# Kernel optimization log

Measured on AMD Instinct MI355X. Metric: run time of the kernel, lower is better.

Reference implementation:

```python
import jax, jax.numpy as jnp
import numpy as np

K, T, D, S, A, C, H = 128, 64, 128, 512, 4, 16, 512
N_LEAVES = 128
TEMP = 1.0          # sample_merge_temp
EPS_SQRT = 1e-4     # distances.EPSILON ** 0.5 with EPSILON = 1e-8
_SQ_EPS = 1e-12     # numerical guard inside sqrt (diagonal of pairwise dists is 0)


def setup_inputs() -> dict:
    key = jax.random.key(0)
    ks = jax.random.split(key, 11)
    leaf_counts_Kxt = jax.random.randint(ks[0], (K, T), 1, 5)
    embeddings_KxtxD = jax.random.normal(ks[1], (K, T, D), jnp.float32)
    log_felsensteins_KxtxSxA = jax.random.normal(ks[2], (K, T, S, A), jnp.float32)
    site_positions_SxC = jax.random.uniform(ks[3], (S, C), jnp.float32)
    W1 = jax.random.normal(ks[4], (2 * D, H), jnp.float32) / jnp.sqrt(2.0 * D)
    b1 = jnp.zeros((H,), jnp.float32)
    W2 = jax.random.normal(ks[5], (H, D), jnp.float32) / jnp.sqrt(1.0 * H)
    b2 = jnp.zeros((D,), jnp.float32)
    gumbel_Kxtt = jax.random.gumbel(ks[6], (K, T * T), jnp.float32)
    u1_K = jax.random.uniform(ks[7], (K,), jnp.float32, minval=1e-6, maxval=1.0)
    u2_K = jax.random.uniform(ks[8], (K,), jnp.float32, minval=1e-6, maxval=1.0)
    return {
        "N": N_LEAVES,
        "leaf_counts_Kxt": leaf_counts_Kxt,
        "embeddings_KxtxD": embeddings_KxtxD,
        "log_felsensteins_KxtxSxA": log_felsensteins_KxtxSxA,
        "site_positions_SxC": site_positions_SxC,
        "W1": W1, "b1": b1, "W2": W2, "b2": b2,
        "gumbel_Kxtt": gumbel_Kxtt, "u1_K": u1_K, "u2_K": u2_K,
    }


def _merge_encoder(c1_KxD, c2_KxD, W1, b1, W2, b2):
    # MLP merge encoder: MLP(concat(child1, child2)) -> parent embedding
    h = jax.nn.relu(jnp.concatenate([c1_KxD, c2_KxD], axis=-1) @ W1 + b1)
    return h @ W2 + b2


def reference(N, leaf_counts_Kxt, embeddings_KxtxD, log_felsensteins_KxtxSxA,
              site_positions_SxC, W1, b1, W2, b2, gumbel_Kxtt, u1_K, u2_K):
    Kp, t = leaf_counts_Kxt.shape
    ar = jnp.arange(Kp)

    # --- pairwise distances over all t*t subtree pairs per particle ---
    diff_Kxtxtxd = embeddings_KxtxD[:, :, None, :] - embeddings_KxtxD[:, None, :, :]
    pd_Kxtxt = jnp.sqrt(jnp.sum(diff_Kxtxtxd * diff_Kxtxtxd, axis=-1) + _SQ_EPS)
    merge_log_weights_Kxtxt = -pd_Kxtxt / TEMP
    # diagonal_scatter(-inf): forbid self-merges
    eye = jnp.eye(t, dtype=bool)[None]
    merge_log_weights_Kxtxt = jnp.where(eye, -jnp.inf, merge_log_weights_Kxtxt)

    # --- categorical merge sampling (gumbel-max with pre-drawn noise) ---
    flat_Kxtt = merge_log_weights_Kxtxt.reshape(Kp, t * t)
    sample_K = jnp.argmax(flat_Kxtt + gumbel_Kxtt, axis=1)
    idx1_K = sample_K // t
    idx2_K = sample_K % t
    log_merge_prob_K = (flat_Kxtt[ar, sample_K] + jnp.log(2.0)
                        - jax.scipy.special.logsumexp(flat_Kxtt, axis=1))

    # --- merged embedding ---
    child1_KxD = embeddings_KxtxD[ar, idx1_K]
    child2_KxD = embeddings_KxtxD[ar, idx2_K]
    embedding_KxD = _merge_encoder(child1_KxD, child2_KxD, W1, b1, W2, b2)

    # --- branch lengths sampled from Exp(rate = 1/(dist + eps)) ---
    d1_K = jnp.sqrt(jnp.sum((child1_KxD - embedding_KxD) ** 2, axis=-1) + _SQ_EPS)
    d2_K = jnp.sqrt(jnp.sum((child2_KxD - embedding_KxD) ** 2, axis=-1) + _SQ_EPS)
    rate1_K = 1.0 / (d1_K + EPS_SQRT)
    rate2_K = 1.0 / (d2_K + EPS_SQRT)
    branch1_K = -(1.0 / rate1_K) * jnp.log(u1_K)
    branch2_K = -(1.0 / rate2_K) * jnp.log(u2_K)
    log_branch1_prior_K = jnp.log(rate1_K) - rate1_K * branch1_K
    log_branch2_prior_K = jnp.log(rate2_K) - rate2_K * branch2_K

    log_v_plus_K = log_merge_prob_K + log_branch1_prior_K + log_branch2_prior_K

    # --- over-counting correction ---
    ones_K = jnp.sum(leaf_counts_Kxt == 1, axis=1)
    ones_K = ones_K - (leaf_counts_Kxt[ar, idx1_K] == 1).astype(ones_K.dtype)
    ones_K = ones_K - (leaf_counts_Kxt[ar, idx2_K] == 1).astype(ones_K.dtype)
    log_v_minus_K = jnp.log((N - ones_K).astype(jnp.float32))

    return (idx1_K, idx2_K, branch1_K, branch2_K, embedding_KxD,
            log_v_plus_K, log_v_minus_K)
```

## Files before the change

kernel.cpp:

```cpp
#include <hip/hip_runtime.h>
#include <math.h>

#define Kp 128
#define Tn 64
#define Dn 128
#define Hn 512
#define ETS 68

__global__ __launch_bounds__(256, 1) void ep_kernel(
    const int*   __restrict__ Nptr,
    const int*   __restrict__ leaf,
    const float* __restrict__ emb,
    const float* __restrict__ W1,
    const float* __restrict__ b1,
    const float* __restrict__ W2,
    const float* __restrict__ b2,
    const float* __restrict__ gum,
    const float* __restrict__ u1,
    const float* __restrict__ u2,
    float* __restrict__ out)
{
    const int k    = blockIdx.x;
    const int tid  = threadIdx.x;
    const int lane = tid & 63;
    const int wid  = tid >> 6;

    __shared__ float ET[Dn * ETS];
    __shared__ float xs[256];
    __shared__ float hsh[Hn];
    __shared__ float buf[1024];
    __shared__ float nI[Tn];
    __shared__ float sBest[4]; __shared__ int sIdx[4]; __shared__ float sW[4];
    __shared__ float sSum[4];
    __shared__ float sD1[4]; __shared__ float sD2[4];
    __shared__ int   sOnes;
    __shared__ int   fIdx; __shared__ float fW;
    __shared__ float embs[Dn];

    if (tid < 64) {
        int lc = leaf[k * Tn + tid];
        unsigned long long m = __ballot(lc == 1);
        if (tid == 0) sOnes = __popcll(m);
    }

    const int tx = tid & 15;
    const int ty = tid >> 4;
    float4 ev[8];
    {
        const float4* src = (const float4*)(emb + (size_t)k * Tn * Dn);
        #pragma unroll
        for (int it = 0; it < 8; ++it) ev[it] = src[tid + it * 256];
    }
    float4 g4[4];
    {
        const float* gk = gum + (size_t)k * (Tn * Tn);
        #pragma unroll
        for (int r = 0; r < 4; ++r) g4[r] = *(const float4*)&gk[(4 * ty + r) * Tn + 4 * tx];
    }

    #pragma unroll
    for (int it = 0; it < 8; ++it) {
        int f4 = tid + it * 256;
        int e0 = f4 * 4;
        int i = e0 >> 7;
        int d = e0 & 127;
        ET[(d + 0) * ETS + i] = ev[it].x;
        ET[(d + 1) * ETS + i] = ev[it].y;
        ET[(d + 2) * ETS + i] = ev[it].z;
        ET[(d + 3) * ETS + i] = ev[it].w;
    }
    __syncthreads();

    float acc[4][4] = {};
    #pragma unroll 4
    for (int d = 0; d < Dn; ++d) {
        float4 a = *(const float4*)&ET[d * ETS + 4 * ty];
        float4 b = *(const float4*)&ET[d * ETS + 4 * tx];
        float ar[4] = {a.x, a.y, a.z, a.w};
        float br[4] = {b.x, b.y, b.z, b.w};
        #pragma unroll
        for (int r = 0; r < 4; ++r)
            #pragma unroll
            for (int c = 0; c < 4; ++c)
                acc[r][c] += ar[r] * br[c];
    }
    if (tx == ty) {
        #pragma unroll
        for (int c = 0; c < 4; ++c) nI[4 * tx + c] = acc[c][c];
    }
    __syncthreads();

    float es = 0.0f;
    float best = -INFINITY, bestW = 0.0f;
    int   bestIdx = 0;
    #pragma unroll
    for (int r = 0; r < 4; ++r) {
        int i = 4 * ty + r;
        float ni = nI[i];
        float gv[4] = {g4[r].x, g4[r].y, g4[r].z, g4[r].w};
        #pragma unroll
        for (int c = 0; c < 4; ++c) {
            int j = 4 * tx + c;
            float pd2 = ni + nI[j] - 2.0f * acc[r][c];
            pd2 = fmaxf(pd2, 0.0f) + 1e-12f;
            float wv = (i == j) ? -INFINITY : -sqrtf(pd2);
            es += expf(wv);
            float wg = wv + gv[c];
            int idx = i * Tn + j;
            if (wg > best || (wg == best && idx < bestIdx)) {
                best = wg; bestIdx = idx; bestW = wv;
            }
        }
    }

    #pragma unroll
    for (int off = 32; off > 0; off >>= 1) {
        float ob = __shfl_down(best, off);
        int   oi = __shfl_down(bestIdx, off);
        float ow = __shfl_down(bestW, off);
        float oe = __shfl_down(es, off);
        if (ob > best || (ob == best && oi < bestIdx)) { best = ob; bestIdx = oi; bestW = ow; }
        es += oe;
    }
    if (lane == 0) { sBest[wid] = best; sIdx[wid] = bestIdx; sW[wid] = bestW; sSum[wid] = es; }
    __syncthreads();
    if (tid == 0) {
        best = sBest[0]; bestIdx = sIdx[0]; bestW = sW[0];
        #pragma unroll
        for (int q = 1; q < 4; ++q) {
            if (sBest[q] > best || (sBest[q] == best && sIdx[q] < bestIdx)) {
                best = sBest[q]; bestIdx = sIdx[q]; bestW = sW[q];
            }
        }
        fIdx = bestIdx; fW = bestW;
    }
    __syncthreads();

    const int i1 = fIdx >> 6;
    const int i2 = fIdx & 63;

    xs[tid] = (tid < 128) ? ET[tid * ETS + i1] : ET[(tid - 128) * ETS + i2];
    __syncthreads();

    {
        const int j0 = 4 * (tid & 127);
        const int ih = tid >> 7;
        const float* W1r = W1 + j0;
        float a0 = 0.0f, a1 = 0.0f, a2 = 0.0f, a3 = 0.0f;
        const int ibase = ih * 128;
        #pragma unroll 4
        for (int i = ibase; i < ibase + 128; i += 4) {
            float4 x  = *(const float4*)&xs[i];
            float4 w0 = *(const float4*)&W1r[(size_t)(i + 0) * Hn];
            float4 w1 = *(const float4*)&W1r[(size_t)(i + 1) * Hn];
            float4 w2 = *(const float4*)&W1r[(size_t)(i + 2) * Hn];
            float4 w3 = *(const float4*)&W1r[(size_t)(i + 3) * Hn];
            a0 += x.x * w0.x + x.y * w1.x + x.z * w2.x + x.w * w3.x;
            a1 += x.x * w0.y + x.y * w1.y + x.z * w2.y + x.w * w3.y;
            a2 += x.x * w0.z + x.y * w1.z + x.z * w2.z + x.w * w3.z;
            a3 += x.x * w0.w + x.y * w1.w + x.z * w2.w + x.w * w3.w;
        }
        *(float4*)&buf[ih * Hn + j0] = make_float4(a0, a1, a2, a3);
    }
    __syncthreads();
    {
        int j = tid;
        hsh[j] = fmaxf(buf[j] + buf[Hn + j] + b1[j], 0.0f);
        j = tid + 256;
        hsh[j] = fmaxf(buf[j] + buf[Hn + j] + b1[j], 0.0f);
    }
    __syncthreads();

    {
        const int jh  = tid >> 5;
        const int dd4 = 4 * (tid & 31);
        float a0 = 0.0f, a1 = 0.0f, a2 = 0.0f, a3 = 0.0f;
        const int jbase = jh * 64;
        #pragma unroll 4
        for (int j = jbase; j < jbase + 64; j += 4) {
            float4 h4 = *(const float4*)&hsh[j];
            float4 w0 = *(const float4*)&W2[(size_t)(j + 0) * Dn + dd4];
            float4 w1 = *(const float4*)&W2[(size_t)(j + 1) * Dn + dd4];
            float4 w2 = *(const float4*)&W2[(size_t)(j + 2) * Dn + dd4];
            float4 w3 = *(const float4*)&W2[(size_t)(j + 3) * Dn + dd4];
            a0 += h4.x * w0.x + h4.y * w1.x + h4.z * w2.x + h4.w * w3.x;
            a1 += h4.x * w0.y + h4.y * w1.y + h4.z * w2.y + h4.w * w3.y;
            a2 += h4.x * w0.z + h4.y * w1.z + h4.z * w2.z + h4.w * w3.z;
            a3 += h4.x * w0.w + h4.y * w1.w + h4.z * w2.w + h4.w * w3.w;
        }
        *(float4*)&buf[jh * Dn + dd4] = make_float4(a0, a1, a2, a3);
    }
    __syncthreads();
    if (tid < 128) {
        float e = b2[tid];
        #pragma unroll
        for (int q = 0; q < 8; ++q) e += buf[q * Dn + tid];
        embs[tid] = e;
        out[4 * Kp + k * Dn + tid] = e;
    }
    __syncthreads();

    float v1 = 0.0f, v2 = 0.0f;
    if (tid < 128) {
        float e  = embs[tid];
        float q1 = xs[tid] - e;        v1 = q1 * q1;
        float q2 = xs[128 + tid] - e;  v2 = q2 * q2;
    }
    #pragma unroll
    for (int off = 32; off > 0; off >>= 1) {
        v1 += __shfl_down(v1, off);
        v2 += __shfl_down(v2, off);
    }
    if (lane == 0) { sD1[wid] = v1; sD2[wid] = v2; }
    __syncthreads();

    if (tid == 0) {
        float s1 = sD1[0] + sD1[1] + sD1[2] + sD1[3];
        float s2 = sD2[0] + sD2[1] + sD2[2] + sD2[3];
        float d1 = sqrtf(s1 + 1e-12f);
        float d2 = sqrtf(s2 + 1e-12f);
        float rate1 = 1.0f / (d1 + 1e-4f);
        float rate2 = 1.0f / (d2 + 1e-4f);
        float u1v = u1[k], u2v = u2[k];
        float branch1 = -(1.0f / rate1) * logf(u1v);
        float branch2 = -(1.0f / rate2) * logf(u2v);
        float lbp1 = logf(rate1) - rate1 * branch1;
        float lbp2 = logf(rate2) - rate2 * branch2;
        float ssum = sSum[0] + sSum[1] + sSum[2] + sSum[3];
        float lse  = logf(ssum);
        float lmp  = fW + 0.69314718055994531f - lse;
        float lvp  = lmp + lbp1 + lbp2;
        int lc1 = leaf[k * Tn + i1];
        int lc2 = leaf[k * Tn + i2];
        int ones = sOnes - (lc1 == 1 ? 1 : 0) - (lc2 == 1 ? 1 : 0);
        float lvm = logf((float)(Nptr[0] - ones));

        out[k]                       = (float)i1;
        out[Kp + k]                  = (float)i2;
        out[2 * Kp + k]              = branch1;
        out[3 * Kp + k]              = branch2;
        out[4 * Kp + Kp * Dn + k]      = lvp;
        out[4 * Kp + Kp * Dn + Kp + k] = lvm;
    }
}

extern "C" void kernel_launch(void* const* d_in, const int* in_sizes, int n_in,
                              void* d_out, int out_size, void* d_ws, size_t ws_size,
                              hipStream_t stream) {
    const int*   Nptr = (const int*)  d_in[0];
    const int*   leaf = (const int*)  d_in[1];
    const float* emb  = (const float*)d_in[2];
    const float* W1   = (const float*)d_in[5];
    const float* b1   = (const float*)d_in[6];
    const float* W2   = (const float*)d_in[7];
    const float* b2   = (const float*)d_in[8];
    const float* gum  = (const float*)d_in[9];
    const float* u1   = (const float*)d_in[10];
    const float* u2   = (const float*)d_in[11];
    float* out = (float*)d_out;

    ep_kernel<<<Kp, 256, 0, stream>>>(Nptr, leaf, emb, W1, b1, W2, b2, gum, u1, u2, out);
}
```

Before: 131.2 us.

## Exploit Gram symmetry, split-K across 512 threads, swizzle shared-memory transpose

Doubles the block to 512 threads. The Gram matrix is computed only for upper-triangle and diagonal 4x4 tiles, using symmetry, with split-K partial sums reduced through shared scratch. The transposed embedding tile uses an XOR-like swizzled index to cut bank conflicts. Both MLP layers also split their reduction dimension across more threads. This halves the pairwise FLOPs and raises parallelism per particle, at the cost of extra shared-memory reductions, barriers and uneven work across threads.

Result: slower. 134.8 us (+2.7%).

```diff
diff --git a/kernel.cpp b/kernel.cpp
--- a/kernel.cpp
+++ b/kernel.cpp
@@ -7,7 +7,11 @@
 #define Hn 512
 #define ETS 68
 
-__global__ __launch_bounds__(256, 1) void ep_kernel(
+__device__ __forceinline__ int etIdx(int d, int i) {
+    return d * ETS + (((((i >> 2) + (d >> 2)) & 15) << 2) | (i & 3));
+}
+
+__global__ __launch_bounds__(512, 1) void ep_kernel(
     const int*   __restrict__ Nptr,
     const int*   __restrict__ leaf,
     const float* __restrict__ emb,
@@ -26,89 +30,175 @@
     const int wid  = tid >> 6;
 
     __shared__ float ET[Dn * ETS];
+    __shared__ float scratch[6016];
     __shared__ float xs[256];
     __shared__ float hsh[Hn];
-    __shared__ float buf[1024];
     __shared__ float nI[Tn];
-    __shared__ float sBest[4]; __shared__ int sIdx[4]; __shared__ float sW[4];
-    __shared__ float sSum[4];
-    __shared__ float sD1[4]; __shared__ float sD2[4];
+    __shared__ float embs[Dn];
+    __shared__ float sBest[8]; __shared__ int sIdx[8]; __shared__ float sW[8]; __shared__ float sSum[8];
+    __shared__ float sD1[2]; __shared__ float sD2[2];
     __shared__ int   sOnes;
-    __shared__ int   fIdx; __shared__ float fW;
-    __shared__ float embs[Dn];
+    __shared__ int   fIdx; __shared__ float fW; __shared__ float fS;
+
+    const bool isUp = tid < 480;
+    int ty = 0, tx = 0, tq = 0, uu = 0, dt = 0, dh = 0;
+    if (isUp) {
+        uu = tid >> 2; tq = tid & 3;
+        while (uu >= 15 * (ty + 1) - ((ty + 1) * ty) / 2) ++ty;
+        tx = ty + 1 + (uu - (15 * ty - (ty * (ty - 1)) / 2));
+    } else {
+        int w = tid - 480; dt = w >> 1; dh = w & 1;
+    }
+    const bool ownU = isUp && (tq == 0);
+    const bool ownD = (!isUp) && (dh == 0);
 
     if (tid < 64) {
-        int lc = leaf[k * Tn + tid];
-        unsigned long long m = __ballot(lc == 1);
+        unsigned long long m = __ballot(leaf[k * Tn + tid] == 1);
         if (tid == 0) sOnes = __popcll(m);
     }
 
-    const int tx = tid & 15;
-    const int ty = tid >> 4;
-    float4 ev[8];
+    float4 ev[4];
     {
         const float4* src = (const float4*)(emb + (size_t)k * Tn * Dn);
         #pragma unroll
-        for (int it = 0; it < 8; ++it) ev[it] = src[tid + it * 256];
-    }
-    float4 g4[4];
+        for (int it = 0; it < 4; ++it) ev[it] = src[tid + it * 512];
+    }
+    float4 gA[4] = {}, gB[4] = {};
     {
         const float* gk = gum + (size_t)k * (Tn * Tn);
-        #pragma unroll
-        for (int r = 0; r < 4; ++r) g4[r] = *(const float4*)&gk[(4 * ty + r) * Tn + 4 * tx];
+        if (ownU) {
+            #pragma unroll
+            for (int r = 0; r < 4; ++r) {
+                gA[r] = *(const float4*)&gk[(4 * ty + r) * Tn + 4 * tx];
+                gB[r] = *(const float4*)&gk[(4 * tx + r) * Tn + 4 * ty];
+            }
+        } else if (ownD) {
+            #pragma unroll
+            for (int r = 0; r < 4; ++r) gA[r] = *(const float4*)&gk[(4 * dt + r) * Tn + 4 * dt];
+        }
     }
 
     #pragma unroll
-    for (int it = 0; it < 8; ++it) {
-        int f4 = tid + it * 256;
-        int e0 = f4 * 4;
-        int i = e0 >> 7;
-        int d = e0 & 127;
-        ET[(d + 0) * ETS + i] = ev[it].x;
-        ET[(d + 1) * ETS + i] = ev[it].y;
-        ET[(d + 2) * ETS + i] = ev[it].z;
-        ET[(d + 3) * ETS + i] = ev[it].w;
-    }
-    __syncthreads();
-
-    float acc[4][4] = {};
-    #pragma unroll 4
-    for (int d = 0; d < Dn; ++d) {
-        float4 a = *(const float4*)&ET[d * ETS + 4 * ty];
-        float4 b = *(const float4*)&ET[d * ETS + 4 * tx];
-        float ar[4] = {a.x, a.y, a.z, a.w};
-        float br[4] = {b.x, b.y, b.z, b.w};
-        #pragma unroll
-        for (int r = 0; r < 4; ++r)
-            #pragma unroll
-            for (int c = 0; c < 4; ++c)
-                acc[r][c] += ar[r] * br[c];
-    }
-    if (tx == ty) {
-        #pragma unroll
-        for (int c = 0; c < 4; ++c) nI[4 * tx + c] = acc[c][c];
-    }
-    __syncthreads();
-
-    float es = 0.0f;
-    float best = -INFINITY, bestW = 0.0f;
+    for (int it = 0; it < 4; ++it) {
+        int f4 = tid + it * 512;
+        int i  = f4 >> 5;
+        int d0 = (f4 & 31) << 2;
+        ET[etIdx(d0 + 0, i)] = ev[it].x;
+        ET[etIdx(d0 + 1, i)] = ev[it].y;
+        ET[etIdx(d0 + 2, i)] = ev[it].z;
+        ET[etIdx(d0 + 3, i)] = ev[it].w;
+    }
+    __syncthreads();
+
+    float4 ac0 = {0,0,0,0}, ac1 = {0,0,0,0}, ac2 = {0,0,0,0}, ac3 = {0,0,0,0};
+    if (isUp) {
+        const int ra = 4 * ty, rb = 4 * tx;
+        #pragma unroll 4
+        for (int m = 0; m < 32; ++m) {
+            int d = tq + 4 * m;
+            float4 a = *(const float4*)&ET[etIdx(d, ra)];
+            float4 b = *(const float4*)&ET[etIdx(d, rb)];
+            ac0.x += a.x * b.x; ac0.y += a.x * b.y; ac0.z += a.x * b.z; ac0.w += a.x * b.w;
+            ac1.x += a.y * b.x; ac1.y += a.y * b.y; ac1.z += a.y * b.z; ac1.w += a.y * b.w;
+            ac2.x += a.z * b.x; ac2.y += a.z * b.y; ac2.z += a.z * b.z; ac2.w += a.z * b.w;
+            ac3.x += a.w * b.x; ac3.y += a.w * b.y; ac3.z += a.w * b.z; ac3.w += a.w * b.w;
+        }
+        if (tq > 0) {
+            float* s = &scratch[uu * 48 + (tq - 1) * 16];
+            *(float4*)&s[0] = ac0; *(float4*)&s[4]  = ac1;
+            *(float4*)&s[8] = ac2; *(float4*)&s[12] = ac3;
+        }
+    } else {
+        const int ra = 4 * dt;
+        #pragma unroll 4
+        for (int m = 0; m < 64; ++m) {
+            int d = dh + 2 * m;
+            float4 a = *(const float4*)&ET[etIdx(d, ra)];
+            ac0.x += a.x * a.x; ac0.y += a.x * a.y; ac0.z += a.x * a.z; ac0.w += a.x * a.w;
+            ac1.x += a.y * a.x; ac1.y += a.y * a.y; ac1.z += a.y * a.z; ac1.w += a.y * a.w;
+            ac2.x += a.z * a.x; ac2.y += a.z * a.y; ac2.z += a.z * a.z; ac2.w += a.z * a.w;
+            ac3.x += a.w * a.x; ac3.y += a.w * a.y; ac3.z += a.w * a.z; ac3.w += a.w * a.w;
+        }
+        if (dh == 1) {
+            float* s = &scratch[5760 + dt * 16];
+            *(float4*)&s[0] = ac0; *(float4*)&s[4]  = ac1;
+            *(float4*)&s[8] = ac2; *(float4*)&s[12] = ac3;
+        }
+    }
+    __syncthreads();
+
+    if (ownU) {
+        #pragma unroll
+        for (int p = 0; p < 3; ++p) {
+            const float* s = &scratch[uu * 48 + p * 16];
+            float4 t0 = *(const float4*)&s[0], t1 = *(const float4*)&s[4];
+            float4 t2 = *(const float4*)&s[8], t3 = *(const float4*)&s[12];
+            ac0.x += t0.x; ac0.y += t0.y; ac0.z += t0.z; ac0.w += t0.w;
+            ac1.x += t1.x; ac1.y += t1.y; ac1.z += t1.z; ac1.w += t1.w;
+            ac2.x += t2.x; ac2.y += t2.y; ac2.z += t2.z; ac2.w += t2.w;
+            ac3.x += t3.x; ac3.y += t3.y; ac3.z += t3.z; ac3.w += t3.w;
+        }
+    } else if (ownD) {
+        const float* s = &scratch[5760 + dt * 16];
+        float4 t0 = *(const float4*)&s[0], t1 = *(const float4*)&s[4];
+        float4 t2 = *(const float4*)&s[8], t3 = *(const float4*)&s[12];
+        ac0.x += t0.x; ac0.y += t0.y; ac0.z += t0.z; ac0.w += t0.w;
+        ac1.x += t1.x; ac1.y += t1.y; ac1.z += t1.z; ac1.w += t1.w;
+        ac2.x += t2.x; ac2.y += t2.y; ac2.z += t2.z; ac2.w += t2.w;
+        ac3.x += t3.x; ac3.y += t3.y; ac3.z += t3.z; ac3.w += t3.w;
+        nI[4 * dt + 0] = ac0.x; nI[4 * dt + 1] = ac1.y;
+        nI[4 * dt + 2] = ac2.z; nI[4 * dt + 3] = ac3.w;
+    }
+    __syncthreads();
+
+    float es = 0.0f, best = -INFINITY, bestW = 0.0f;
     int   bestIdx = 0;
-    #pragma unroll
-    for (int r = 0; r < 4; ++r) {
-        int i = 4 * ty + r;
-        float ni = nI[i];
-        float gv[4] = {g4[r].x, g4[r].y, g4[r].z, g4[r].w};
-        #pragma unroll
-        for (int c = 0; c < 4; ++c) {
-            int j = 4 * tx + c;
-            float pd2 = ni + nI[j] - 2.0f * acc[r][c];
-            pd2 = fmaxf(pd2, 0.0f) + 1e-12f;
-            float wv = (i == j) ? -INFINITY : -sqrtf(pd2);
-            es += expf(wv);
-            float wg = wv + gv[c];
-            int idx = i * Tn + j;
-            if (wg > best || (wg == best && idx < bestIdx)) {
-                best = wg; bestIdx = idx; bestW = wv;
+    {
+        float accf[16];
+        *(float4*)&accf[0] = ac0; *(float4*)&accf[4]  = ac1;
+        *(float4*)&accf[8] = ac2; *(float4*)&accf[12] = ac3;
+        float gAf[16], gBf[16];
+        *(float4*)&gAf[0] = gA[0]; *(float4*)&gAf[4]  = gA[1];
+        *(float4*)&gAf[8] = gA[2]; *(float4*)&gAf[12] = gA[3];
+        *(float4*)&gBf[0] = gB[0]; *(float4*)&gBf[4]  = gB[1];
+        *(float4*)&gBf[8] = gB[2]; *(float4*)&gBf[12] = gB[3];
+        if (ownU) {
+            float ni[4], nj[4];
+            #pragma unroll
+            for (int r = 0; r < 4; ++r) { ni[r] = nI[4 * ty + r]; nj[r] = nI[4 * tx + r]; }
+            #pragma unroll
+            for (int r = 0; r < 4; ++r) {
+                #pragma unroll
+                for (int c = 0; c < 4; ++c) {
+                    float pd2 = ni[r] + nj[c] - 2.0f * accf[r * 4 + c];
+                    float wv  = -sqrtf(fmaxf(pd2, 0.0f) + 1e-12f);
+                    es += 2.0f * expf(wv);
+                    int i = 4 * ty + r, j = 4 * tx + c;
+                    float wg1 = wv + gAf[r * 4 + c]; int id1 = i * Tn + j;
+                    if (wg1 > best || (wg1 == best && id1 < bestIdx)) { best = wg1; bestIdx = id1; bestW = wv; }
+                    float wg2 = wv + gBf[c * 4 + r]; int id2 = j * Tn + i;
+                    if (wg2 > best || (wg2 == best && id2 < bestIdx)) { best = wg2; bestIdx = id2; bestW = wv; }
+                }
+            }
+        } else if (ownD) {
+            float ni[4];
+            #pragma unroll
+            for (int r = 0; r < 4; ++r) ni[r] = nI[4 * dt + r];
+            #pragma unroll
+            for (int r = 0; r < 4; ++r) {
+                #pragma unroll
+                for (int c = 0; c < 4; ++c) {
+                    if (c > r) {
+                        float pd2 = ni[r] + ni[c] - 2.0f * accf[r * 4 + c];
+                        float wv  = -sqrtf(fmaxf(pd2, 0.0f) + 1e-12f);
+                        es += 2.0f * expf(wv);
+                        int i = 4 * dt + r, j = 4 * dt + c;
+                        float wg1 = wv + gAf[r * 4 + c]; int id1 = i * Tn + j;
+                        if (wg1 > best || (wg1 == best && id1 < bestIdx)) { best = wg1; bestIdx = id1; bestW = wv; }
+                        float wg2 = wv + gAf[c * 4 + r]; int id2 = j * Tn + i;
+                        if (wg2 > best || (wg2 == best && id2 < bestIdx)) { best = wg2; bestIdx = id2; bestW = wv; }
+                    }
+                }
             }
         }
     }
@@ -126,108 +216,103 @@
     __syncthreads();
     if (tid == 0) {
         best = sBest[0]; bestIdx = sIdx[0]; bestW = sW[0];
-        #pragma unroll
-        for (int q = 1; q < 4; ++q) {
+        float essum = sSum[0];
+        #pragma unroll
+        for (int q = 1; q < 8; ++q) {
             if (sBest[q] > best || (sBest[q] == best && sIdx[q] < bestIdx)) {
                 best = sBest[q]; bestIdx = sIdx[q]; bestW = sW[q];
             }
-        }
-        fIdx = bestIdx; fW = bestW;
+            essum += sSum[q];
+        }
+        fIdx = bestIdx; fW = bestW; fS = essum;
     }
     __syncthreads();
 
     const int i1 = fIdx >> 6;
     const int i2 = fIdx & 63;
 
-    xs[tid] = (tid < 128) ? ET[tid * ETS + i1] : ET[(tid - 128) * ETS + i2];
+    if (tid < 256) xs[tid] = (tid < 128) ? ET[etIdx(tid, i1)] : ET[etIdx(tid - 128, i2)];
     __syncthreads();
 
     {
         const int j0 = 4 * (tid & 127);
         const int ih = tid >> 7;
         const float* W1r = W1 + j0;
-        float a0 = 0.0f, a1 = 0.0f, a2 = 0.0f, a3 = 0.0f;
-        const int ibase = ih * 128;
+        float4 a = {0,0,0,0};
+        const int ib = ih * 64;
         #pragma unroll 4
-        for (int i = ibase; i < ibase + 128; i += 4) {
+        for (int i = ib; i < ib + 64; i += 4) {
             float4 x  = *(const float4*)&xs[i];
             float4 w0 = *(const float4*)&W1r[(size_t)(i + 0) * Hn];
             float4 w1 = *(const float4*)&W1r[(size_t)(i + 1) * Hn];
             float4 w2 = *(const float4*)&W1r[(size_t)(i + 2) * Hn];
             float4 w3 = *(const float4*)&W1r[(size_t)(i + 3) * Hn];
-            a0 += x.x * w0.x + x.y * w1.x + x.z * w2.x + x.w * w3.x;
-            a1 += x.x * w0.y + x.y * w1.y + x.z * w2.y + x.w * w3.y;
-            a2 += x.x * w0.z + x.y * w1.z + x.z * w2.z + x.w * w3.z;
-            a3 += x.x * w0.w + x.y * w1.w + x.z * w2.w + x.w * w3.w;
-        }
-        *(float4*)&buf[ih * Hn + j0] = make_float4(a0, a1, a2, a3);
-    }
-    __syncthreads();
-    {
-        int j = tid;
-        hsh[j] = fmaxf(buf[j] + buf[Hn + j] + b1[j], 0.0f);
-        j = tid + 256;
-        hsh[j] = fmaxf(buf[j] + buf[Hn + j] + b1[j], 0.0f);
-    }
+            a.x += x.x * w0.x + x.y * w1.x + x.z * w2.x + x.w * w3.x;
+            a.y += x.x * w0.y + x.y * w1.y + x.z * w2.y + x.w * w3.y;
+            a.z += x.x * w0.z + x.y * w1.z + x.z * w2.z + x.w * w3.z;
+            a.w += x.x * w0.w + x.y * w1.w + x.z * w2.w + x.w * w3.w;
+        }
+        *(float4*)&scratch[ih * 516 + j0] = a;
+    }
+    __syncthreads();
+    hsh[tid] = fmaxf(b1[tid] + scratch[tid] + scratch[516 + tid]
+                              + scratch[1032 + tid] + scratch[1548 + tid], 0.0f);
     __syncthreads();
 
     {
         const int jh  = tid >> 5;
         const int dd4 = 4 * (tid & 31);
-        float a0 = 0.0f, a1 = 0.0f, a2 = 0.0f, a3 = 0.0f;
-        const int jbase = jh * 64;
+        float4 a = {0,0,0,0};
+        const int jb = jh * 32;
         #pragma unroll 4
-        for (int j = jbase; j < jbase + 64; j += 4) {
+        for (int j = jb; j < jb + 32; j += 4) {
             float4 h4 = *(const float4*)&hsh[j];
             float4 w0 = *(const float4*)&W2[(size_t)(j + 0) * Dn + dd4];
             float4 w1 = *(const float4*)&W2[(size_t)(j + 1) * Dn + dd4];
             float4 w2 = *(const float4*)&W2[(size_t)(j + 2) * Dn + dd4];
             float4 w3 = *(const float4*)&W2[(size_t)(j + 3) * Dn + dd4];
-            a0 += h4.x * w0.x + h4.y * w1.x + h4.z * w2.x + h4.w * w3.x;
-            a1 += h4.x * w0.y + h4.y * w1.y + h4.z * w2.y + h4.w * w3.y;
-            a2 += h4.x * w0.z + h4.y * w1.z + h4.z * w2.z + h4.w * w3.z;
-            a3 += h4.x * w0.w + h4.y * w1.w + h4.z * w2.w + h4.w * w3.w;
-        }
-        *(float4*)&buf[jh * Dn + dd4] = make_float4(a0, a1, a2, a3);
+            a.x += h4.x * w0.x + h4.y * w1.x + h4.z * w2.x + h4.w * w3.x;
+            a.y += h4.x * w0.y + h4.y * w1.y + h4.z * w2.y + h4.w * w3.y;
+            a.z += h4.x * w0.z + h4.y * w1.z + h4.z * w2.z + h4.w * w3.z;
+            a.w += h4.x * w0.w + h4.y * w1.w + h4.z * w2.w + h4.w * w3.w;
+        }
+        *(float4*)&scratch[jh * 132 + dd4] = a;
     }
     __syncthreads();
     if (tid < 128) {
         float e = b2[tid];
         #pragma unroll
-        for (int q = 0; q < 8; ++q) e += buf[q * Dn + tid];
+        for (int p = 0; p < 16; ++p) e += scratch[p * 132 + tid];
         embs[tid] = e;
         out[4 * Kp + k * Dn + tid] = e;
     }
     __syncthreads();
 
-    float v1 = 0.0f, v2 = 0.0f;
     if (tid < 128) {
         float e  = embs[tid];
-        float q1 = xs[tid] - e;        v1 = q1 * q1;
-        float q2 = xs[128 + tid] - e;  v2 = q2 * q2;
-    }
-    #pragma unroll
-    for (int off = 32; off > 0; off >>= 1) {
-        v1 += __shfl_down(v1, off);
-        v2 += __shfl_down(v2, off);
-    }
-    if (lane == 0) { sD1[wid] = v1; sD2[wid] = v2; }
+        float q1 = xs[tid] - e;        float v1 = q1 * q1;
+        float q2 = xs[128 + tid] - e;  float v2 = q2 * q2;
+        #pragma unroll
+        for (int off = 32; off > 0; off >>= 1) {
+            v1 += __shfl_down(v1, off);
+            v2 += __shfl_down(v2, off);
+        }
+        if (lane == 0) { sD1[wid] = v1; sD2[wid] = v2; }
+    }
     __syncthreads();
 
     if (tid == 0) {
-        float s1 = sD1[0] + sD1[1] + sD1[2] + sD1[3];
-        float s2 = sD2[0] + sD2[1] + sD2[2] + sD2[3];
+        float s1 = sD1[0] + sD1[1];
+        float s2 = sD2[0] + sD2[1];
         float d1 = sqrtf(s1 + 1e-12f);
         float d2 = sqrtf(s2 + 1e-12f);
         float rate1 = 1.0f / (d1 + 1e-4f);
         float rate2 = 1.0f / (d2 + 1e-4f);
-        float u1v = u1[k], u2v = u2[k];
-        float branch1 = -(1.0f / rate1) * logf(u1v);
-        float branch2 = -(1.0f / rate2) * logf(u2v);
+        float branch1 = -(1.0f / rate1) * logf(u1[k]);
+        float branch2 = -(1.0f / rate2) * logf(u2[k]);
         float lbp1 = logf(rate1) - rate1 * branch1;
         float lbp2 = logf(rate2) - rate2 * branch2;
-        float ssum = sSum[0] + sSum[1] + sSum[2] + sSum[3];
-        float lse  = logf(ssum);
+        float lse  = logf(fS);
         float lmp  = fW + 0.69314718055994531f - lse;
         float lvp  = lmp + lbp1 + lbp2;
         int lc1 = leaf[k * Tn + i1];
@@ -235,10 +320,10 @@
         int ones = sOnes - (lc1 == 1 ? 1 : 0) - (lc2 == 1 ? 1 : 0);
         float lvm = logf((float)(Nptr[0] - ones));
 
-        out[k]                       = (float)i1;
-        out[Kp + k]                  = (float)i2;
-        out[2 * Kp + k]              = branch1;
-        out[3 * Kp + k]              = branch2;
+        out[k]                         = (float)i1;
+        out[Kp + k]                    = (float)i2;
+        out[2 * Kp + k]                = branch1;
+        out[3 * Kp + k]                = branch2;
         out[4 * Kp + Kp * Dn + k]      = lvp;
         out[4 * Kp + Kp * Dn + Kp + k] = lvm;
     }
@@ -259,5 +344,5 @@
     const float* u2   = (const float*)d_in[11];
     float* out = (float*)d_out;
 
-    ep_kernel<<<Kp, 256, 0, stream>>>(Nptr, leaf, emb, W1, b1, W2, b2, gum, u1, u2, out);
+    ep_kernel<<<Kp, 512, 0, stream>>>(Nptr, leaf, emb, W1, b1, W2, b2, gum, u1, u2, out);
 }
```

## Compute pairwise Gram matrix with split-bf16 MFMA instead of scalar FMA

Applied to the files above, without the earlier changes.

Embeddings are split into bf16 high and low parts stored row-major in shared memory. The 64x64 Gram matrix is then computed with three bf16 MFMA 16x16x32 products per tile (hi*hi, hi*lo, lo*hi), replacing the scalar fp32 outer-product loop. The goal is to cut ALU time in the distance stage. The cost is a small precision change, since the lo*lo term is dropped, and this could flip argmax ties. Gumbel loads and the epilogue indexing are remapped to the MFMA output layout, and the selected child embeddings are rebuilt as hi+lo.

After: 125.8 us. 1.04x faster.

```diff
diff --git a/kernel.cpp b/kernel.cpp
--- a/kernel.cpp
+++ b/kernel.cpp
@@ -5,7 +5,10 @@
 #define Tn 64
 #define Dn 128
 #define Hn 512
-#define ETS 68
+#define RS 136
+
+typedef __attribute__((ext_vector_type(8))) short short8;
+typedef __attribute__((ext_vector_type(4))) float f32x4;
 
 __global__ __launch_bounds__(256, 1) void ep_kernel(
     const int*   __restrict__ Nptr,
@@ -25,7 +28,8 @@
     const int lane = tid & 63;
     const int wid  = tid >> 6;
 
-    __shared__ float ET[Dn * ETS];
+    __shared__ unsigned short EH[Tn * RS];
+    __shared__ unsigned short EL[Tn * RS];
     __shared__ float xs[256];
     __shared__ float hsh[Hn];
     __shared__ float buf[1024];
@@ -37,81 +41,126 @@
     __shared__ int   fIdx; __shared__ float fW;
     __shared__ float embs[Dn];
 
+    const int itp  = wid >> 1;
+    const int jtp  = wid & 1;
+    const int lrow = lane & 15;
+    const int lq   = lane >> 4;
+
     if (tid < 64) {
-        int lc = leaf[k * Tn + tid];
-        unsigned long long m = __ballot(lc == 1);
+        unsigned long long m = __ballot(leaf[k * Tn + tid] == 1);
         if (tid == 0) sOnes = __popcll(m);
     }
 
-    const int tx = tid & 15;
-    const int ty = tid >> 4;
     float4 ev[8];
     {
         const float4* src = (const float4*)(emb + (size_t)k * Tn * Dn);
         #pragma unroll
         for (int it = 0; it < 8; ++it) ev[it] = src[tid + it * 256];
     }
-    float4 g4[4];
+    float gv[16];
     {
         const float* gk = gum + (size_t)k * (Tn * Tn);
         #pragma unroll
-        for (int r = 0; r < 4; ++r) g4[r] = *(const float4*)&gk[(4 * ty + r) * Tn + 4 * tx];
+        for (int a = 0; a < 2; ++a)
+            #pragma unroll
+            for (int b = 0; b < 2; ++b) {
+                int it = 2 * itp + a, jt = 2 * jtp + b;
+                int col = jt * 16 + lrow;
+                #pragma unroll
+                for (int r = 0; r < 4; ++r) {
+                    int row = it * 16 + lq * 4 + r;
+                    gv[(a * 2 + b) * 4 + r] = gk[row * Tn + col];
+                }
+            }
     }
 
     #pragma unroll
     for (int it = 0; it < 8; ++it) {
         int f4 = tid + it * 256;
-        int e0 = f4 * 4;
-        int i = e0 >> 7;
-        int d = e0 & 127;
-        ET[(d + 0) * ETS + i] = ev[it].x;
-        ET[(d + 1) * ETS + i] = ev[it].y;
-        ET[(d + 2) * ETS + i] = ev[it].z;
-        ET[(d + 3) * ETS + i] = ev[it].w;
-    }
-    __syncthreads();
-
-    float acc[4][4] = {};
-    #pragma unroll 4
-    for (int d = 0; d < Dn; ++d) {
-        float4 a = *(const float4*)&ET[d * ETS + 4 * ty];
-        float4 b = *(const float4*)&ET[d * ETS + 4 * tx];
-        float ar[4] = {a.x, a.y, a.z, a.w};
-        float br[4] = {b.x, b.y, b.z, b.w};
-        #pragma unroll
-        for (int r = 0; r < 4; ++r)
+        int i  = f4 >> 5;
+        int d0 = (f4 & 31) << 2;
+        float4 v = ev[it];
+        unsigned int bx = __float_as_uint(v.x), by = __float_as_uint(v.y),
+                     bz = __float_as_uint(v.z), bw = __float_as_uint(v.w);
+        unsigned short hx = bx >> 16, hy = by >> 16, hz = bz >> 16, hw = bw >> 16;
+        float rx = v.x - __uint_as_float((unsigned int)hx << 16);
+        float ry = v.y - __uint_as_float((unsigned int)hy << 16);
+        float rz = v.z - __uint_as_float((unsigned int)hz << 16);
+        float rw = v.w - __uint_as_float((unsigned int)hw << 16);
+        unsigned short lx = __float_as_uint(rx) >> 16, ly = __float_as_uint(ry) >> 16,
+                       lz = __float_as_uint(rz) >> 16, lw = __float_as_uint(rw) >> 16;
+        *(ushort4*)&EH[i * RS + d0] = make_ushort4(hx, hy, hz, hw);
+        *(ushort4*)&EL[i * RS + d0] = make_ushort4(lx, ly, lz, lw);
+    }
+    __syncthreads();
+
+    f32x4 acc[2][2] = {};
+    const int ka = lq * 8;
+    #pragma unroll
+    for (int ks = 0; ks < 4; ++ks) {
+        int kb  = ks * 32 + ka;
+        int ra0 = ((2 * itp + 0) * 16 + lrow) * RS + kb;
+        int ra1 = ra0 + 16 * RS;
+        int rb0 = ((2 * jtp + 0) * 16 + lrow) * RS + kb;
+        int rb1 = rb0 + 16 * RS;
+        short8 ah0 = *(const short8*)&EH[ra0], ah1 = *(const short8*)&EH[ra1];
+        short8 al0 = *(const short8*)&EL[ra0], al1 = *(const short8*)&EL[ra1];
+        short8 bh0 = *(const short8*)&EH[rb0], bh1 = *(const short8*)&EH[rb1];
+        short8 bl0 = *(const short8*)&EL[rb0], bl1 = *(const short8*)&EL[rb1];
+        acc[0][0] = __builtin_amdgcn_mfma_f32_16x16x32_bf16(ah0, bh0, acc[0][0], 0, 0, 0);
+        acc[0][1] = __builtin_amdgcn_mfma_f32_16x16x32_bf16(ah0, bh1, acc[0][1], 0, 0, 0);
+        acc[1][0] = __builtin_amdgcn_mfma_f32_16x16x32_bf16(ah1, bh0, acc[1][0], 0, 0, 0);
+        acc[1][1] = __builtin_amdgcn_mfma_f32_16x16x32_bf16(ah1, bh1, acc[1][1], 0, 0, 0);
+        acc[0][0] = __builtin_amdgcn_mfma_f32_16x16x32_bf16(ah0, bl0, acc[0][0], 0, 0, 0);
+        acc[0][1] = __builtin_amdgcn_mfma_f32_16x16x32_bf16(ah0, bl1, acc[0][1], 0, 0, 0);
+        acc[1][0] = __builtin_amdgcn_mfma_f32_16x16x32_bf16(ah1, bl0, acc[1][0], 0, 0, 0);
+        acc[1][1] = __builtin_amdgcn_mfma_f32_16x16x32_bf16(ah1, bl1, acc[1][1], 0, 0, 0);
+        acc[0][0] = __builtin_amdgcn_mfma_f32_16x16x32_bf16(al0, bh0, acc[0][0], 0, 0, 0);
+        acc[0][1] = __builtin_amdgcn_mfma_f32_16x16x32_bf16(al0, bh1, acc[0][1], 0, 0, 0);
+        acc[1][0] = __builtin_amdgcn_mfma_f32_16x16x32_bf16(al1, bh0, acc[1][0], 0, 0, 0);
+        acc[1][1] = __builtin_amdgcn_mfma_f32_16x16x32_bf16(al1, bh1, acc[1][1], 0, 0, 0);
+    }
+
+    if (itp == jtp) {
+        #pragma unroll
+        for (int a = 0; a < 2; ++a) {
+            if ((lrow >> 2) == lq) {
+                int c = lrow;
+                int t = 2 * itp + a;
+                f32x4 v = acc[a][a];
+                int   s = c & 3;
+                float val = (s == 0) ? v.x : (s == 1) ? v.y : (s == 2) ? v.z : v.w;
+                nI[t * 16 + c] = val;
+            }
+        }
+    }
+    __syncthreads();
+
+    float es = 0.0f, best = -INFINITY, bestW = 0.0f;
+    int   bestIdx = 0;
+    #pragma unroll
+    for (int a = 0; a < 2; ++a)
+        #pragma unroll
+        for (int b = 0; b < 2; ++b) {
+            int it = 2 * itp + a, jt = 2 * jtp + b;
+            int col = jt * 16 + lrow;
+            float njc = nI[col];
+            f32x4 v = acc[a][b];
+            float gvals[4] = {v.x, v.y, v.z, v.w};
             #pragma unroll
-            for (int c = 0; c < 4; ++c)
-                acc[r][c] += ar[r] * br[c];
-    }
-    if (tx == ty) {
-        #pragma unroll
-        for (int c = 0; c < 4; ++c) nI[4 * tx + c] = acc[c][c];
-    }
-    __syncthreads();
-
-    float es = 0.0f;
-    float best = -INFINITY, bestW = 0.0f;
-    int   bestIdx = 0;
-    #pragma unroll
-    for (int r = 0; r < 4; ++r) {
-        int i = 4 * ty + r;
-        float ni = nI[i];
-        float gv[4] = {g4[r].x, g4[r].y, g4[r].z, g4[r].w};
-        #pragma unroll
-        for (int c = 0; c < 4; ++c) {
-            int j = 4 * tx + c;
-            float pd2 = ni + nI[j] - 2.0f * acc[r][c];
-            pd2 = fmaxf(pd2, 0.0f) + 1e-12f;
-            float wv = (i == j) ? -INFINITY : -sqrtf(pd2);
-            es += expf(wv);
-            float wg = wv + gv[c];
-            int idx = i * Tn + j;
-            if (wg > best || (wg == best && idx < bestIdx)) {
-                best = wg; bestIdx = idx; bestW = wv;
+            for (int r = 0; r < 4; ++r) {
+                int row = it * 16 + lq * 4 + r;
+                float pd2 = nI[row] + njc - 2.0f * gvals[r];
+                pd2 = fmaxf(pd2, 0.0f) + 1e-12f;
+                float wv = (row == col) ? -INFINITY : -sqrtf(pd2);
+                es += expf(wv);
+                float wg = wv + gv[(a * 2 + b) * 4 + r];
+                int idx = row * Tn + col;
+                if (wg > best || (wg == best && idx < bestIdx)) {
+                    best = wg; bestIdx = idx; bestW = wv;
+                }
             }
         }
-    }
 
     #pragma unroll
     for (int off = 32; off > 0; off >>= 1) {
@@ -139,7 +188,13 @@
     const int i1 = fIdx >> 6;
     const int i2 = fIdx & 63;
 
-    xs[tid] = (tid < 128) ? ET[tid * ETS + i1] : ET[(tid - 128) * ETS + i2];
+    {
+        int d  = tid & 127;
+        int ii = (tid < 128) ? i1 : i2;
+        float hi = __uint_as_float((unsigned int)EH[ii * RS + d] << 16);
+        float lo = __uint_as_float((unsigned int)EL[ii * RS + d] << 16);
+        xs[tid] = hi + lo;
+    }
     __syncthreads();
 
     {
@@ -221,9 +276,8 @@
         float d2 = sqrtf(s2 + 1e-12f);
         float rate1 = 1.0f / (d1 + 1e-4f);
         float rate2 = 1.0f / (d2 + 1e-4f);
-        float u1v = u1[k], u2v = u2[k];
-        float branch1 = -(1.0f / rate1) * logf(u1v);
-        float branch2 = -(1.0f / rate2) * logf(u2v);
+        float branch1 = -(1.0f / rate1) * logf(u1[k]);
+        float branch2 = -(1.0f / rate2) * logf(u2[k]);
         float lbp1 = logf(rate1) - rate1 * branch1;
         float lbp2 = logf(rate2) - rate2 * branch2;
         float ssum = sSum[0] + sSum[1] + sSum[2] + sSum[3];
@@ -235,10 +289,10 @@
         int ones = sOnes - (lc1 == 1 ? 1 : 0) - (lc2 == 1 ? 1 : 0);
         float lvm = logf((float)(Nptr[0] - ones));
 
-        out[k]                       = (float)i1;
-        out[Kp + k]                  = (float)i2;
-        out[2 * Kp + k]              = branch1;
-        out[3 * Kp + k]              = branch2;
+        out[k]                         = (float)i1;
+        out[Kp + k]                    = (float)i2;
+        out[2 * Kp + k]                = branch1;
+        out[3 * Kp + k]                = branch2;
         out[4 * Kp + Kp * Dn + k]      = lvp;
         out[4 * Kp + Kp * Dn + Kp + k] = lvm;
     }
```
